# Kernel tuning notes

Measured on AMD Instinct MI355X. Metric: run time of the kernel, lower is better.

## Reference

```python
import jax, jax.numpy as jnp
import numpy as np

B, IN, OUT, G = 64, 8192, 8192, 64
NG = IN // G  # groups per row


def setup_inputs() -> dict:
    key = jax.random.key(0)
    k1, k2, k3, k4 = jax.random.split(key, 4)
    x = jax.random.normal(k1, (B, IN), dtype=jnp.float32)
    # packed 2-bit codes: 4 codes per byte, LSB-first (matches _pack2)
    w_packed = jax.random.randint(k2, (OUT, IN // 4), 0, 256, dtype=jnp.int32).astype(jnp.uint8)
    # scales from _calc_group_qparams are positive (max_abs/1.5); zp is always 2
    scales = jax.random.uniform(k3, (OUT, NG), dtype=jnp.float32, minval=0.01, maxval=0.1)
    zps = jnp.full((OUT, NG), 2, dtype=jnp.int32)
    bias = jax.random.normal(k4, (OUT,), dtype=jnp.float32) * 0.01
    return {"x": x, "w_packed": w_packed, "scales": scales, "zps": zps, "bias": bias}


def _dequant(w_packed, scales, zps):
    # unpack: byte -> 4 two-bit codes, LSB first (matches _unpack2)
    out_f = w_packed.shape[0]
    codes = jnp.stack([(w_packed >> s) & 3 for s in (0, 2, 4, 6)], axis=-1)  # [OUT, IN//4, 4]
    q = codes.reshape(out_f, NG, G).astype(jnp.int32)                        # [OUT, NG, G]
    # per-group dequant: (q - zp) * scale
    w = (q - zps[:, :, None]).astype(jnp.float32) * scales[:, :, None]
    return w.reshape(out_f, IN)                                              # [OUT, IN]


def reference(x, w_packed, scales, zps, bias):
    w = _dequant(w_packed, scales, zps)  # [OUT, IN] fp32
    # original accumulates xg @ wg.T per group; equivalent to full x @ w.T
    return x @ w.T + bias                # [B, OUT]
```

## Files before the change

### kernel.cpp

```cpp
#include <hip/hip_runtime.h>
#include <hip/hip_bf16.h>

#define B_    64
#define IN_   8192
#define OUT_  8192
#define NG_   128
#define PB_   2048

#define KSPLIT 16
#define KC     512
#define CGS    4

typedef float f32x4 __attribute__((ext_vector_type(4)));
typedef short s16x8 __attribute__((ext_vector_type(8)));

union FU { float f; unsigned u; };

__global__ __launch_bounds__(256) void k_pre(const float* __restrict__ x,
                                             const float* __restrict__ bias,
                                             __hip_bfloat16* __restrict__ xb,
                                             float* __restrict__ out) {
    const int bid = blockIdx.x;
    if (bid < 512) {
        int i = (bid * 256 + threadIdx.x) * 4;
        float4 f = *(const float4*)(x + i);
        __hip_bfloat162 h0 = __float22bfloat162_rn(make_float2(f.x, f.y));
        __hip_bfloat162 h1 = __float22bfloat162_rn(make_float2(f.z, f.w));
        uint2 o; o.x = *(unsigned*)&h0; o.y = *(unsigned*)&h1;
        *(uint2*)(xb + i) = o;
    } else {
        int i = ((bid - 512) * 256 + threadIdx.x) * 4;
        *(float4*)(out + i) = *(const float4*)(bias + (i & (OUT_ - 1)));
    }
}

__global__ __launch_bounds__(256, 2) void k_main(
    const __hip_bfloat16* __restrict__ xb,
    const unsigned char* __restrict__ wp,
    const float* __restrict__ scales,
    const int* __restrict__ zps,
    float* __restrict__ out)
{
    __shared__ uint4 x_lds[4096];
    __shared__ int wflag, zflag;

    const int tid  = threadIdx.x;
    const int wave = tid >> 6;
    const int lane = tid & 63;
    const int q    = lane >> 4;
    const int nn   = lane & 15;

    const int bid     = blockIdx.x;
    const int kidx    = bid & (KSPLIT - 1);
    const int nblk    = bid >> 4;
    const int kbase   = kidx * KC;
    const int colbase = nblk * 256 + wave * 64;

#pragma unroll
    for (int i = 0; i < 16; ++i) {
        int sg = wave * 16 + i;
        int sb = sg >> 4, b = (sg >> 2) & 3, mt = sg & 3;
        const __hip_bfloat16* src =
            xb + (mt * 16 + nn) * IN_ + kbase + sb * 128 + q * 32 + b * 8;
        unsigned int* dst = (unsigned int*)((char*)x_lds + sg * 1024);
        __builtin_amdgcn_global_load_lds(
            (const __attribute__((address_space(1))) unsigned int*)src,
            (__attribute__((address_space(3))) unsigned int*)dst, 16, 0, 0);
    }

    unsigned wv = ((const unsigned int*)wp)[tid];
    int      zv = zps[tid];
    if (tid == 0) { wflag = 0; zflag = 0; }
    __syncthreads();
    if (wv > 255u) wflag = 1;
    if (zv != 2)   zflag = 1;
    __syncthreads();
    const bool u8mode = (wflag != 0);
    const bool zgen   = (zflag != 0);

    uint2 w8[4][CGS];
    const int wb = (kbase >> 2) + q * 8;
    if (u8mode) {
#pragma unroll
        for (int sb = 0; sb < 4; ++sb)
#pragma unroll
            for (int cg = 0; cg < CGS; ++cg) {
                int n = colbase + cg * 16 + nn;
                w8[sb][cg] = *(const uint2*)(wp + n * PB_ + wb + sb * 32);
            }
    } else {
        const int* wpi = (const int*)wp;
#pragma unroll
        for (int sb = 0; sb < 4; ++sb)
#pragma unroll
            for (int cg = 0; cg < CGS; ++cg) {
                int n = colbase + cg * 16 + nn;
                const int* p = wpi + n * PB_ + wb + sb * 32;
                uint4 a  = *(const uint4*)p;
                uint4 b2 = *(const uint4*)(p + 4);
                w8[sb][cg].x = __builtin_amdgcn_perm(a.y,  a.x,  0x0C0C0400) |
                               __builtin_amdgcn_perm(a.w,  a.z,  0x04000C0C);
                w8[sb][cg].y = __builtin_amdgcn_perm(b2.y, b2.x, 0x0C0C0400) |
                               __builtin_amdgcn_perm(b2.w, b2.z, 0x04000C0C);
            }
    }

    float sf[4][CGS], fb[4][CGS];
#pragma unroll
    for (int sb = 0; sb < 4; ++sb)
#pragma unroll
        for (int cg = 0; cg < CGS; ++cg) {
            int n = colbase + cg * 16 + nn;
            int g = kidx * 8 + sb * 2 + (q >> 1);
            float s = scales[n * NG_ + g] * 1.001953125f;
            float zpf = zgen ? (float)zps[n * NG_ + g] : 2.0f;
            sf[sb][cg] = s;
            fb[sb][cg] = -zpf * s;
        }

    f32x4 acc[CGS][4];
#pragma unroll
    for (int cg = 0; cg < CGS; ++cg)
#pragma unroll
        for (int mt = 0; mt < 4; ++mt)
            acc[cg][mt] = (f32x4){0.f, 0.f, 0.f, 0.f};

#pragma unroll
    for (int sb = 0; sb < 4; ++sb) {
#pragma unroll
        for (int dw = 0; dw < 2; ++dw) {
#pragma unroll
            for (int h = 0; h < 2; ++h) {
                const int b = dw * 2 + h;
                union { uint4 u4; s16x8 s8; } av[4];
#pragma unroll
                for (int mt = 0; mt < 4; ++mt)
                    av[mt].u4 = x_lds[((sb * 4 + b) * 4 + mt) * 64 + lane];
#pragma unroll
                for (int cg = 0; cg < CGS; ++cg) {
                    const unsigned v = dw ? w8[sb][cg].y : w8[sb][cg].x;
                    const float s = sf[sb][cg], fbv = fb[sb][cg];
                    union { unsigned u[4]; s16x8 s8; } bf;
#pragma unroll
                    for (int m = 0; m < 4; ++m) {
                        const int sh = h * 16 + m * 4;
                        FU f0, f1;
                        f0.f = fmaf((float)((v >> sh) & 3u), s, fbv);
                        f1.f = fmaf((float)((v >> (sh + 2)) & 3u), s, fbv);
                        bf.u[m] = __builtin_amdgcn_perm(f1.u, f0.u, 0x07060302);
                    }
#pragma unroll
                    for (int mt = 0; mt < 4; ++mt)
                        acc[cg][mt] = __builtin_amdgcn_mfma_f32_16x16x32_bf16(
                            av[mt].s8, bf.s8, acc[cg][mt], 0, 0, 0);
                }
            }
        }
    }

#pragma unroll
    for (int cg = 0; cg < CGS; ++cg) {
        const int col = colbase + cg * 16 + nn;
#pragma unroll
        for (int mt = 0; mt < 4; ++mt)
#pragma unroll
            for (int r = 0; r < 4; ++r)
                atomicAdd(out + (mt * 16 + q * 4 + r) * OUT_ + col, acc[cg][mt][r]);
    }
}

extern "C" void kernel_launch(void* const* d_in, const int* in_sizes, int n_in,
                              void* d_out, int out_size, void* d_ws, size_t ws_size,
                              hipStream_t stream) {
    const float*         x      = (const float*)d_in[0];
    const unsigned char* wp     = (const unsigned char*)d_in[1];
    const float*         scales = (const float*)d_in[2];
    const int*           zps    = (const int*)d_in[3];
    const float*         bias   = (const float*)d_in[4];
    float*               out    = (float*)d_out;

    __hip_bfloat16* xb = (__hip_bfloat16*)d_ws;

    k_pre<<<1024, 256, 0, stream>>>(x, bias, xb, out);
    k_main<<<512, 256, 0, stream>>>(xb, wp, scales, zps, out);
}
```

Measured before the change: 133.5 us.

## Halve split-K with per-block two-phase K loop and deterministic partial-sum reduction

```diff
diff --git a/kernel.cpp b/kernel.cpp
--- a/kernel.cpp
+++ b/kernel.cpp
@@ -7,31 +7,22 @@
 #define NG_   128
 #define PB_   2048
 
-#define KSPLIT 16
-#define KC     512
-#define CGS    4
+#define KSPLIT 8
+#define KC     1024
+#define CGS    2
 
 typedef float f32x4 __attribute__((ext_vector_type(4)));
 typedef short s16x8 __attribute__((ext_vector_type(8)));
-
 union FU { float f; unsigned u; };
 
 __global__ __launch_bounds__(256) void k_pre(const float* __restrict__ x,
-                                             const float* __restrict__ bias,
-                                             __hip_bfloat16* __restrict__ xb,
-                                             float* __restrict__ out) {
-    const int bid = blockIdx.x;
-    if (bid < 512) {
-        int i = (bid * 256 + threadIdx.x) * 4;
-        float4 f = *(const float4*)(x + i);
-        __hip_bfloat162 h0 = __float22bfloat162_rn(make_float2(f.x, f.y));
-        __hip_bfloat162 h1 = __float22bfloat162_rn(make_float2(f.z, f.w));
-        uint2 o; o.x = *(unsigned*)&h0; o.y = *(unsigned*)&h1;
-        *(uint2*)(xb + i) = o;
-    } else {
-        int i = ((bid - 512) * 256 + threadIdx.x) * 4;
-        *(float4*)(out + i) = *(const float4*)(bias + (i & (OUT_ - 1)));
-    }
+                                             __hip_bfloat16* __restrict__ xb) {
+    int i = (blockIdx.x * 256 + threadIdx.x) * 4;
+    float4 f = *(const float4*)(x + i);
+    __hip_bfloat162 h0 = __float22bfloat162_rn(make_float2(f.x, f.y));
+    __hip_bfloat162 h1 = __float22bfloat162_rn(make_float2(f.z, f.w));
+    uint2 o; o.x = *(unsigned*)&h0; o.y = *(unsigned*)&h1;
+    *(uint2*)(xb + i) = o;
 }
 
 __global__ __launch_bounds__(256, 2) void k_main(
@@ -39,7 +30,7 @@
     const unsigned char* __restrict__ wp,
     const float* __restrict__ scales,
     const int* __restrict__ zps,
-    float* __restrict__ out)
+    float* __restrict__ part)
 {
     __shared__ uint4 x_lds[4096];
     __shared__ int wflag, zflag;
@@ -52,9 +43,9 @@
 
     const int bid     = blockIdx.x;
     const int kidx    = bid & (KSPLIT - 1);
-    const int nblk    = bid >> 4;
+    const int nblk    = bid >> 3;
     const int kbase   = kidx * KC;
-    const int colbase = nblk * 256 + wave * 64;
+    const int colbase = nblk * 128 + wave * 32;
 
 #pragma unroll
     for (int i = 0; i < 16; ++i) {
@@ -78,45 +69,52 @@
     const bool u8mode = (wflag != 0);
     const bool zgen   = (zflag != 0);
 
-    uint2 w8[4][CGS];
+    uint2 w8[2][4][CGS];
     const int wb = (kbase >> 2) + q * 8;
     if (u8mode) {
 #pragma unroll
+        for (int ph = 0; ph < 2; ++ph)
+#pragma unroll
+            for (int sb = 0; sb < 4; ++sb)
+#pragma unroll
+                for (int cg = 0; cg < CGS; ++cg) {
+                    int n = colbase + cg * 16 + nn;
+                    w8[ph][sb][cg] =
+                        *(const uint2*)(wp + n * PB_ + wb + ph * 128 + sb * 32);
+                }
+    } else {
+        const int* wpi = (const int*)wp;
+#pragma unroll
+        for (int ph = 0; ph < 2; ++ph)
+#pragma unroll
+            for (int sb = 0; sb < 4; ++sb)
+#pragma unroll
+                for (int cg = 0; cg < CGS; ++cg) {
+                    int n = colbase + cg * 16 + nn;
+                    const int* p = wpi + n * PB_ + wb + ph * 128 + sb * 32;
+                    uint4 a  = *(const uint4*)p;
+                    uint4 b2 = *(const uint4*)(p + 4);
+                    w8[ph][sb][cg].x = __builtin_amdgcn_perm(a.y,  a.x,  0x0C0C0400) |
+                                       __builtin_amdgcn_perm(a.w,  a.z,  0x04000C0C);
+                    w8[ph][sb][cg].y = __builtin_amdgcn_perm(b2.y, b2.x, 0x0C0C0400) |
+                                       __builtin_amdgcn_perm(b2.w, b2.z, 0x04000C0C);
+                }
+    }
+
+    float sf[2][4][CGS], fb[2][4][CGS];
+#pragma unroll
+    for (int ph = 0; ph < 2; ++ph)
+#pragma unroll
         for (int sb = 0; sb < 4; ++sb)
 #pragma unroll
             for (int cg = 0; cg < CGS; ++cg) {
                 int n = colbase + cg * 16 + nn;
-                w8[sb][cg] = *(const uint2*)(wp + n * PB_ + wb + sb * 32);
+                int g = kidx * 16 + ph * 8 + sb * 2 + (q >> 1);
+                float s = scales[n * NG_ + g] * 1.001953125f;
+                float zpf = zgen ? (float)zps[n * NG_ + g] : 2.0f;
+                sf[ph][sb][cg] = s;
+                fb[ph][sb][cg] = -zpf * s;
             }
-    } else {
-        const int* wpi = (const int*)wp;
-#pragma unroll
-        for (int sb = 0; sb < 4; ++sb)
-#pragma unroll
-            for (int cg = 0; cg < CGS; ++cg) {
-                int n = colbase + cg * 16 + nn;
-                const int* p = wpi + n * PB_ + wb + sb * 32;
-                uint4 a  = *(const uint4*)p;
-                uint4 b2 = *(const uint4*)(p + 4);
-                w8[sb][cg].x = __builtin_amdgcn_perm(a.y,  a.x,  0x0C0C0400) |
-                               __builtin_amdgcn_perm(a.w,  a.z,  0x04000C0C);
-                w8[sb][cg].y = __builtin_amdgcn_perm(b2.y, b2.x, 0x0C0C0400) |
-                               __builtin_amdgcn_perm(b2.w, b2.z, 0x04000C0C);
-            }
-    }
-
-    float sf[4][CGS], fb[4][CGS];
-#pragma unroll
-    for (int sb = 0; sb < 4; ++sb)
-#pragma unroll
-        for (int cg = 0; cg < CGS; ++cg) {
-            int n = colbase + cg * 16 + nn;
-            int g = kidx * 8 + sb * 2 + (q >> 1);
-            float s = scales[n * NG_ + g] * 1.001953125f;
-            float zpf = zgen ? (float)zps[n * NG_ + g] : 2.0f;
-            sf[sb][cg] = s;
-            fb[sb][cg] = -zpf * s;
-        }
 
     f32x4 acc[CGS][4];
 #pragma unroll
@@ -126,38 +124,57 @@
             acc[cg][mt] = (f32x4){0.f, 0.f, 0.f, 0.f};
 
 #pragma unroll
-    for (int sb = 0; sb < 4; ++sb) {
-#pragma unroll
-        for (int dw = 0; dw < 2; ++dw) {
-#pragma unroll
-            for (int h = 0; h < 2; ++h) {
-                const int b = dw * 2 + h;
-                union { uint4 u4; s16x8 s8; } av[4];
-#pragma unroll
-                for (int mt = 0; mt < 4; ++mt)
-                    av[mt].u4 = x_lds[((sb * 4 + b) * 4 + mt) * 64 + lane];
-#pragma unroll
-                for (int cg = 0; cg < CGS; ++cg) {
-                    const unsigned v = dw ? w8[sb][cg].y : w8[sb][cg].x;
-                    const float s = sf[sb][cg], fbv = fb[sb][cg];
-                    union { unsigned u[4]; s16x8 s8; } bf;
-#pragma unroll
-                    for (int m = 0; m < 4; ++m) {
-                        const int sh = h * 16 + m * 4;
-                        FU f0, f1;
-                        f0.f = fmaf((float)((v >> sh) & 3u), s, fbv);
-                        f1.f = fmaf((float)((v >> (sh + 2)) & 3u), s, fbv);
-                        bf.u[m] = __builtin_amdgcn_perm(f1.u, f0.u, 0x07060302);
+    for (int ph = 0; ph < 2; ++ph) {
+        if (ph) {
+            __syncthreads();
+#pragma unroll
+            for (int i = 0; i < 16; ++i) {
+                int sg = wave * 16 + i;
+                int sb = sg >> 4, b = (sg >> 2) & 3, mt = sg & 3;
+                const __hip_bfloat16* src = xb + (mt * 16 + nn) * IN_ +
+                    kbase + 512 + sb * 128 + q * 32 + b * 8;
+                unsigned int* dst = (unsigned int*)((char*)x_lds + sg * 1024);
+                __builtin_amdgcn_global_load_lds(
+                    (const __attribute__((address_space(1))) unsigned int*)src,
+                    (__attribute__((address_space(3))) unsigned int*)dst, 16, 0, 0);
+            }
+            __syncthreads();
+        }
+#pragma unroll
+        for (int sb = 0; sb < 4; ++sb) {
+#pragma unroll
+            for (int dw = 0; dw < 2; ++dw) {
+#pragma unroll
+                for (int h = 0; h < 2; ++h) {
+                    const int b = dw * 2 + h;
+                    union { uint4 u4; s16x8 s8; } av[4];
+#pragma unroll
+                    for (int mt = 0; mt < 4; ++mt)
+                        av[mt].u4 = x_lds[((sb * 4 + b) * 4 + mt) * 64 + lane];
+#pragma unroll
+                    for (int cg = 0; cg < CGS; ++cg) {
+                        const unsigned v = dw ? w8[ph][sb][cg].y : w8[ph][sb][cg].x;
+                        const float s = sf[ph][sb][cg], fbv = fb[ph][sb][cg];
+                        union { unsigned u[4]; s16x8 s8; } bf;
+#pragma unroll
+                        for (int m = 0; m < 4; ++m) {
+                            const int sh = h * 16 + m * 4;
+                            FU f0, f1;
+                            f0.f = fmaf((float)((v >> sh) & 3u), s, fbv);
+                            f1.f = fmaf((float)((v >> (sh + 2)) & 3u), s, fbv);
+                            bf.u[m] = __builtin_amdgcn_perm(f1.u, f0.u, 0x07060302);
+                        }
+#pragma unroll
+                        for (int mt = 0; mt < 4; ++mt)
+                            acc[cg][mt] = __builtin_amdgcn_mfma_f32_16x16x32_bf16(
+                                av[mt].s8, bf.s8, acc[cg][mt], 0, 0, 0);
                     }
-#pragma unroll
-                    for (int mt = 0; mt < 4; ++mt)
-                        acc[cg][mt] = __builtin_amdgcn_mfma_f32_16x16x32_bf16(
-                            av[mt].s8, bf.s8, acc[cg][mt], 0, 0, 0);
                 }
             }
         }
     }
 
+    float* pp = part + kidx * (B_ * OUT_);
 #pragma unroll
     for (int cg = 0; cg < CGS; ++cg) {
         const int col = colbase + cg * 16 + nn;
@@ -165,8 +182,21 @@
         for (int mt = 0; mt < 4; ++mt)
 #pragma unroll
             for (int r = 0; r < 4; ++r)
-                atomicAdd(out + (mt * 16 + q * 4 + r) * OUT_ + col, acc[cg][mt][r]);
-    }
+                pp[(mt * 16 + q * 4 + r) * OUT_ + col] = acc[cg][mt][r];
+    }
+}
+
+__global__ __launch_bounds__(256) void k_reduce(const float* __restrict__ part,
+                                                const float* __restrict__ bias,
+                                                float* __restrict__ out) {
+    int i = (blockIdx.x * 256 + threadIdx.x) * 4;
+    float4 s = *(const float4*)(bias + (i & (OUT_ - 1)));
+#pragma unroll
+    for (int p = 0; p < KSPLIT; ++p) {
+        float4 v = *(const float4*)(part + p * (B_ * OUT_) + i);
+        s.x += v.x; s.y += v.y; s.z += v.z; s.w += v.w;
+    }
+    *(float4*)(out + i) = s;
 }
 
 extern "C" void kernel_launch(void* const* d_in, const int* in_sizes, int n_in,
@@ -179,8 +209,10 @@
     const float*         bias   = (const float*)d_in[4];
     float*               out    = (float*)d_out;
 
-    __hip_bfloat16* xb = (__hip_bfloat16*)d_ws;
-
-    k_pre<<<1024, 256, 0, stream>>>(x, bias, xb, out);
-    k_main<<<512, 256, 0, stream>>>(xb, wp, scales, zps, out);
-}
+    __hip_bfloat16* xb   = (__hip_bfloat16*)d_ws;
+    float*          part = (float*)((char*)d_ws + (1 << 20));
+
+    k_pre<<<512, 256, 0, stream>>>(x, xb);
+    k_main<<<512, 256, 0, stream>>>(xb, wp, scales, zps, part);
+    k_reduce<<<512, 256, 0, stream>>>(part, bias, out);
+}
```

Measured after the change: 131.0 us. Within noise of the previous version (-1.9%).

## Replace atomic split-K with fp16 partials plus reduce kernel; LUT-based dequant via perm

Applied to the files above, without the earlier changes.

```diff
diff --git a/kernel.cpp b/kernel.cpp
--- a/kernel.cpp
+++ b/kernel.cpp
@@ -6,32 +6,21 @@
 #define OUT_  8192
 #define NG_   128
 #define PB_   2048
-
 #define KSPLIT 16
-#define KC     512
-#define CGS    4
+#define KC    512
 
 typedef float f32x4 __attribute__((ext_vector_type(4)));
 typedef short s16x8 __attribute__((ext_vector_type(8)));
-
-union FU { float f; unsigned u; };
+typedef _Float16 f16x4 __attribute__((ext_vector_type(4)));
 
 __global__ __launch_bounds__(256) void k_pre(const float* __restrict__ x,
-                                             const float* __restrict__ bias,
-                                             __hip_bfloat16* __restrict__ xb,
-                                             float* __restrict__ out) {
-    const int bid = blockIdx.x;
-    if (bid < 512) {
-        int i = (bid * 256 + threadIdx.x) * 4;
-        float4 f = *(const float4*)(x + i);
-        __hip_bfloat162 h0 = __float22bfloat162_rn(make_float2(f.x, f.y));
-        __hip_bfloat162 h1 = __float22bfloat162_rn(make_float2(f.z, f.w));
-        uint2 o; o.x = *(unsigned*)&h0; o.y = *(unsigned*)&h1;
-        *(uint2*)(xb + i) = o;
-    } else {
-        int i = ((bid - 512) * 256 + threadIdx.x) * 4;
-        *(float4*)(out + i) = *(const float4*)(bias + (i & (OUT_ - 1)));
-    }
+                                             __hip_bfloat16* __restrict__ xb) {
+    int i = (blockIdx.x * 256 + threadIdx.x) * 4;
+    float4 f = *(const float4*)(x + i);
+    __hip_bfloat162 h0 = __float22bfloat162_rn(make_float2(f.x, f.y));
+    __hip_bfloat162 h1 = __float22bfloat162_rn(make_float2(f.z, f.w));
+    uint2 o; o.x = *(unsigned*)&h0; o.y = *(unsigned*)&h1;
+    *(uint2*)(xb + i) = o;
 }
 
 __global__ __launch_bounds__(256, 2) void k_main(
@@ -39,7 +28,7 @@
     const unsigned char* __restrict__ wp,
     const float* __restrict__ scales,
     const int* __restrict__ zps,
-    float* __restrict__ out)
+    _Float16* __restrict__ part)
 {
     __shared__ uint4 x_lds[4096];
     __shared__ int wflag, zflag;
@@ -50,24 +39,42 @@
     const int q    = lane >> 4;
     const int nn   = lane & 15;
 
-    const int bid     = blockIdx.x;
-    const int kidx    = bid & (KSPLIT - 1);
-    const int nblk    = bid >> 4;
+    const int kidx    = blockIdx.x & (KSPLIT - 1);
+    const int nblk    = blockIdx.x >> 4;
     const int kbase   = kidx * KC;
     const int colbase = nblk * 256 + wave * 64;
 
+    uint4 w4[4][2];
+    {
+        const unsigned char* wb = wp + (kbase >> 2) + q * 32;
+#pragma unroll
+        for (int cg = 0; cg < 4; ++cg) {
+            const int n = colbase + cg * 16 + nn;
+            w4[cg][0] = *(const uint4*)(wb + n * PB_);
+            w4[cg][1] = *(const uint4*)(wb + n * PB_ + 16);
+        }
+    }
+    float sgl[4][2];
+#pragma unroll
+    for (int cg = 0; cg < 4; ++cg) {
+        const int n = colbase + cg * 16 + nn;
+#pragma unroll
+        for (int sp = 0; sp < 2; ++sp)
+            sgl[cg][sp] = scales[n * NG_ + kidx * 8 + q * 2 + sp];
+    }
 #pragma unroll
     for (int i = 0; i < 16; ++i) {
-        int sg = wave * 16 + i;
-        int sb = sg >> 4, b = (sg >> 2) & 3, mt = sg & 3;
+        const int sg = wave * 16 + i;
+        const int t = sg >> 2, mt = sg & 3;
+        const int sb = t >> 2, b = t & 3;
         const __hip_bfloat16* src =
-            xb + (mt * 16 + nn) * IN_ + kbase + sb * 128 + q * 32 + b * 8;
-        unsigned int* dst = (unsigned int*)((char*)x_lds + sg * 1024);
+            xb + (mt * 16 + nn) * IN_ + kbase + q * 128 + sb * 32 + b * 8;
         __builtin_amdgcn_global_load_lds(
             (const __attribute__((address_space(1))) unsigned int*)src,
-            (__attribute__((address_space(3))) unsigned int*)dst, 16, 0, 0);
-    }
-
+            (__attribute__((address_space(3))) unsigned int*)
+                ((char*)x_lds + sg * 1024),
+            16, 0, 0);
+    }
     unsigned wv = ((const unsigned int*)wp)[tid];
     int      zv = zps[tid];
     if (tid == 0) { wflag = 0; zflag = 0; }
@@ -78,49 +85,47 @@
     const bool u8mode = (wflag != 0);
     const bool zgen   = (zflag != 0);
 
-    uint2 w8[4][CGS];
-    const int wb = (kbase >> 2) + q * 8;
-    if (u8mode) {
-#pragma unroll
-        for (int sb = 0; sb < 4; ++sb)
-#pragma unroll
-            for (int cg = 0; cg < CGS; ++cg) {
-                int n = colbase + cg * 16 + nn;
-                w8[sb][cg] = *(const uint2*)(wp + n * PB_ + wb + sb * 32);
+    if (!u8mode) {
+        const int* wpi = (const int*)wp;
+#pragma unroll
+        for (int cg = 0; cg < 4; ++cg) {
+            const int n = colbase + cg * 16 + nn;
+            const int* p = wpi + n * PB_ + (kbase >> 2) + q * 32;
+#pragma unroll
+            for (int c = 0; c < 2; ++c) {
+                unsigned d[4];
+#pragma unroll
+                for (int dd = 0; dd < 4; ++dd) {
+                    const int* pq = p + c * 16 + dd * 4;
+                    d[dd] = (unsigned)(pq[0] & 0xFF) | ((unsigned)(pq[1] & 0xFF) << 8)
+                          | ((unsigned)(pq[2] & 0xFF) << 16) | ((unsigned)(pq[3] & 0xFF) << 24);
+                }
+                w4[cg][c] = (uint4){d[0], d[1], d[2], d[3]};
             }
-    } else {
-        const int* wpi = (const int*)wp;
-#pragma unroll
-        for (int sb = 0; sb < 4; ++sb)
-#pragma unroll
-            for (int cg = 0; cg < CGS; ++cg) {
-                int n = colbase + cg * 16 + nn;
-                const int* p = wpi + n * PB_ + wb + sb * 32;
-                uint4 a  = *(const uint4*)p;
-                uint4 b2 = *(const uint4*)(p + 4);
-                w8[sb][cg].x = __builtin_amdgcn_perm(a.y,  a.x,  0x0C0C0400) |
-                               __builtin_amdgcn_perm(a.w,  a.z,  0x04000C0C);
-                w8[sb][cg].y = __builtin_amdgcn_perm(b2.y, b2.x, 0x0C0C0400) |
-                               __builtin_amdgcn_perm(b2.w, b2.z, 0x04000C0C);
+        }
+    }
+
+    unsigned tabL[4][2], tabH[4][2];
+#pragma unroll
+    for (int cg = 0; cg < 4; ++cg)
+#pragma unroll
+        for (int sp = 0; sp < 2; ++sp) {
+            const float s = sgl[cg][sp];
+            float zf = 2.0f;
+            if (zgen) {
+                const int n = colbase + cg * 16 + nn;
+                zf = (float)zps[n * NG_ + kidx * 8 + q * 2 + sp];
             }
-    }
-
-    float sf[4][CGS], fb[4][CGS];
-#pragma unroll
-    for (int sb = 0; sb < 4; ++sb)
-#pragma unroll
-        for (int cg = 0; cg < CGS; ++cg) {
-            int n = colbase + cg * 16 + nn;
-            int g = kidx * 8 + sb * 2 + (q >> 1);
-            float s = scales[n * NG_ + g] * 1.001953125f;
-            float zpf = zgen ? (float)zps[n * NG_ + g] : 2.0f;
-            sf[sb][cg] = s;
-            fb[sb][cg] = -zpf * s;
-        }
-
-    f32x4 acc[CGS][4];
-#pragma unroll
-    for (int cg = 0; cg < CGS; ++cg)
+            const float v0 = -zf * s, v1 = v0 + s, v2 = v1 + s, v3 = v2 + s;
+            __hip_bfloat162 lo = __float22bfloat162_rn(make_float2(v0, v1));
+            __hip_bfloat162 hi = __float22bfloat162_rn(make_float2(v2, v3));
+            tabL[cg][sp] = *(unsigned*)&lo;
+            tabH[cg][sp] = *(unsigned*)&hi;
+        }
+
+    f32x4 acc[4][4];
+#pragma unroll
+    for (int cg = 0; cg < 4; ++cg)
 #pragma unroll
         for (int mt = 0; mt < 4; ++mt)
             acc[cg][mt] = (f32x4){0.f, 0.f, 0.f, 0.f};
@@ -128,45 +133,62 @@
 #pragma unroll
     for (int sb = 0; sb < 4; ++sb) {
 #pragma unroll
-        for (int dw = 0; dw < 2; ++dw) {
-#pragma unroll
-            for (int h = 0; h < 2; ++h) {
-                const int b = dw * 2 + h;
-                union { uint4 u4; s16x8 s8; } av[4];
+        for (int b = 0; b < 4; ++b) {
+            const int t = sb * 4 + b;
+            union { uint4 u4; s16x8 s8; } av[4];
+#pragma unroll
+            for (int mt = 0; mt < 4; ++mt)
+                av[mt].u4 = x_lds[(t * 4 + mt) * 64 + lane];
+#pragma unroll
+            for (int cg = 0; cg < 4; ++cg) {
+                const uint4 ch = w4[cg][sb >> 1];
+                const unsigned dwv =
+                    ((const unsigned*)&ch)[((sb & 1) << 1) | (b >> 1)];
+                const unsigned u = (b & 1) ? (dwv >> 16) : (dwv & 0xFFFFu);
+                const unsigned tl = tabL[cg][sb >> 1], th = tabH[cg][sb >> 1];
+                union { unsigned w[4]; s16x8 s8; } bf;
+#pragma unroll
+                for (int m = 0; m < 4; ++m) {
+                    const unsigned c0 = (u >> (4 * m)) & 3u;
+                    const unsigned c1 = (u >> (4 * m + 2)) & 3u;
+                    const unsigned sel = (0x0100u + c0 * 0x0202u)
+                                       | ((0x0100u + c1 * 0x0202u) << 16);
+                    bf.w[m] = __builtin_amdgcn_perm(th, tl, sel);
+                }
 #pragma unroll
                 for (int mt = 0; mt < 4; ++mt)
-                    av[mt].u4 = x_lds[((sb * 4 + b) * 4 + mt) * 64 + lane];
-#pragma unroll
-                for (int cg = 0; cg < CGS; ++cg) {
-                    const unsigned v = dw ? w8[sb][cg].y : w8[sb][cg].x;
-                    const float s = sf[sb][cg], fbv = fb[sb][cg];
-                    union { unsigned u[4]; s16x8 s8; } bf;
-#pragma unroll
-                    for (int m = 0; m < 4; ++m) {
-                        const int sh = h * 16 + m * 4;
-                        FU f0, f1;
-                        f0.f = fmaf((float)((v >> sh) & 3u), s, fbv);
-                        f1.f = fmaf((float)((v >> (sh + 2)) & 3u), s, fbv);
-                        bf.u[m] = __builtin_amdgcn_perm(f1.u, f0.u, 0x07060302);
-                    }
-#pragma unroll
-                    for (int mt = 0; mt < 4; ++mt)
-                        acc[cg][mt] = __builtin_amdgcn_mfma_f32_16x16x32_bf16(
-                            av[mt].s8, bf.s8, acc[cg][mt], 0, 0, 0);
-                }
+                    acc[cg][mt] = __builtin_amdgcn_mfma_f32_16x16x32_bf16(
+                        av[mt].s8, bf.s8, acc[cg][mt], 0, 0, 0);
             }
         }
     }
 
-#pragma unroll
-    for (int cg = 0; cg < CGS; ++cg) {
+    _Float16* pp = part + kidx * (B_ * OUT_);
+#pragma unroll
+    for (int cg = 0; cg < 4; ++cg) {
         const int col = colbase + cg * 16 + nn;
 #pragma unroll
         for (int mt = 0; mt < 4; ++mt)
 #pragma unroll
             for (int r = 0; r < 4; ++r)
-                atomicAdd(out + (mt * 16 + q * 4 + r) * OUT_ + col, acc[cg][mt][r]);
-    }
+                pp[(mt * 16 + q * 4 + r) * OUT_ + col] = (_Float16)acc[cg][mt][r];
+    }
+}
+
+__global__ __launch_bounds__(256) void k_reduce(const _Float16* __restrict__ part,
+                                                const float* __restrict__ bias,
+                                                float* __restrict__ out) {
+    const int gtid = blockIdx.x * 256 + threadIdx.x;
+    const int b  = gtid >> 11;
+    const int n0 = (gtid & 2047) * 4;
+    float4 s = *(const float4*)(bias + n0);
+#pragma unroll
+    for (int p = 0; p < KSPLIT; ++p) {
+        f16x4 v = *(const f16x4*)(part + p * (B_ * OUT_) + b * OUT_ + n0);
+        s.x += (float)v[0]; s.y += (float)v[1];
+        s.z += (float)v[2]; s.w += (float)v[3];
+    }
+    *(float4*)(out + b * OUT_ + n0) = s;
 }
 
 extern "C" void kernel_launch(void* const* d_in, const int* in_sizes, int n_in,
@@ -179,8 +201,10 @@
     const float*         bias   = (const float*)d_in[4];
     float*               out    = (float*)d_out;
 
-    __hip_bfloat16* xb = (__hip_bfloat16*)d_ws;
-
-    k_pre<<<1024, 256, 0, stream>>>(x, bias, xb, out);
-    k_main<<<512, 256, 0, stream>>>(xb, wp, scales, zps, out);
-}
+    __hip_bfloat16* xb   = (__hip_bfloat16*)d_ws;
+    _Float16*       part = (_Float16*)((char*)d_ws + (1 << 20));
+
+    k_pre<<<512, 256, 0, stream>>>(x, xb);
+    k_main<<<512, 256, 0, stream>>>(xb, wp, scales, zps, part);
+    k_reduce<<<512, 256, 0, stream>>>(part, bias, out);
+}
```

Result: no change. 133.0 us (-0.4%).
